# Performance work log

Measured on AMD Instinct MI355X. Metric: run time of the kernel, lower is better.

## Reference

```python
import jax, jax.numpy as jnp
import numpy as np

B, N, D = 2, 4096, 1152   # batch, tokens, txt_dim == pix_dim (num_heads = 1)
RMS_EPS = 1e-8


def setup_inputs() -> dict:
    key = jax.random.key(0)
    ks = jax.random.split(key, 8)
    w = lambda k, shape: jax.random.normal(k, shape, dtype=jnp.float32) * 0.02
    return {
        "x": jax.random.normal(ks[0], (B, N, D), dtype=jnp.float32),
        "c": jax.random.normal(ks[1], (B, N, D), dtype=jnp.float32),
        "Wqkv_pix": w(ks[2], (3 * D, D)),      # nn.Linear(pix_dim, 3*pix_dim), no bias
        "Wqkv_text": w(ks[3], (3 * D, D)),     # nn.Linear(txt_dim, 3*txt_dim), no bias
        "sq_text": jnp.ones((D,), jnp.float32),
        "sk_text": jnp.ones((D,), jnp.float32),
        "sq_pix": jnp.ones((D,), jnp.float32),
        "sk_pix": jnp.ones((D,), jnp.float32),
        "Wproj_pix": w(ks[4], (D, 2 * D)),     # nn.Linear(dim, txt_dim)
        "bproj_pix": jnp.zeros((D,), jnp.float32),
        "Wproj_text": w(ks[5], (D, 2 * D)),    # nn.Linear(dim, pix_dim)
        "bproj_text": jnp.zeros((D,), jnp.float32),
    }


def _rms_norm(t, scale):
    # RMSNorm with p<0 path: L2 norm over last dim, rms = ||x|| * d^-0.5
    d = t.shape[-1]
    rms = jnp.linalg.norm(t, axis=-1, keepdims=True) * (d ** -0.5)
    return scale * (t / (rms + RMS_EPS))


def reference(x, c, Wqkv_pix, Wqkv_text, sq_text, sk_text, sq_pix, sk_pix,
              Wproj_pix, bproj_pix, Wproj_text, bproj_text):
    Bx, Nx, D1 = x.shape  # num_heads == 1, so (B, 1, N, d) == (B, N, d)
    # pix stream QKV (from x)
    qkv_pix = (x @ Wqkv_pix.T).reshape(Bx, Nx, 3, D1)
    q_pix, k_pix, v_pix = qkv_pix[:, :, 0], qkv_pix[:, :, 1], qkv_pix[:, :, 2]
    q_pix = _rms_norm(q_pix, sq_pix)
    k_pix = _rms_norm(k_pix, sk_pix)
    # text stream QKV: NOTE the original code applies qkv_text to x, not c
    qkv_text = (x @ Wqkv_text.T).reshape(Bx, Nx, 3, D1)
    q_text, k_text, v_text = qkv_text[:, :, 0], qkv_text[:, :, 1], qkv_text[:, :, 2]
    q_text = _rms_norm(q_text, sq_text)
    k_text = _rms_norm(k_text, sk_text)
    # concat text/pix along feature dim -> (B, N, 2D)
    q = jnp.concatenate([q_text, q_pix], axis=-1)
    k = jnp.concatenate([k_text, k_pix], axis=-1)
    v = jnp.concatenate([v_text, v_pix], axis=-1)
    scale = (2 * D1) ** -0.5  # head_dim = (txt_dim + pix_dim) / num_heads
    attn = jax.nn.softmax(jnp.einsum("bnd,bmd->bnm", q, k) * scale, axis=-1)
    z = jnp.einsum("bnm,bmd->bnd", attn, v)  # (B, N, 2D)
    x_out = z @ Wproj_pix.T + bproj_pix
    c_out = z @ Wproj_text.T + bproj_text
    return (x_out, c_out)
```

## Files before the change

kernel.cpp:

```cpp
#include <hip/hip_runtime.h>
#include <hip/hip_bf16.h>
#include <stdint.h>

using short8 = __attribute__((ext_vector_type(8))) short;
using f32x4  = __attribute__((ext_vector_type(4))) float;

#define DD 1152
#define ROW 6912

static __device__ __forceinline__ float bf2f(uint32_t h){
  union { uint32_t u; float f; } v; v.u = (h & 0xffffu) << 16; return v.f;
}
static __device__ __forceinline__ ushort f2bf(float f){
  union { float f; uint32_t u; } v; v.f = f;
  uint32_t r = (v.u + 0x7fffu + ((v.u >> 16) & 1u)) >> 16;
  return (ushort)r;
}
static __device__ __forceinline__ uint32_t pack2(float a, float b){
  return (uint32_t)f2bf(a) | ((uint32_t)f2bf(b) << 16);
}

static __device__ __forceinline__ void gload16(const void* g, void* l){
  __builtin_amdgcn_global_load_lds(
      (const __attribute__((address_space(1))) void*)g,
      (__attribute__((address_space(3))) void*)l, 16, 0, 0);
}

template<int EPI>
__global__ __launch_bounds__(512, 2)
void gemm256(const ushort* __restrict__ A, int lda,
             const ushort* __restrict__ Bm, int ldb,
             void* __restrict__ Cout, int ldc,
             int K, float alpha, int ntx, int row0,
             float* __restrict__ out0, float* __restrict__ out1,
             const float* __restrict__ bias0, const float* __restrict__ bias1)
{
  __shared__ __align__(16) ushort lds[65536];
  const int tid  = threadIdx.x;
  const int w    = tid >> 6, lane = tid & 63;
  const int wr   = w >> 2, wc = w & 3;

  const int nwg = gridDim.x;
  const int wg  = blockIdx.x;
  const int swz = (wg & 7) * (nwg >> 3) + (wg >> 3);
  const int tx = swz % ntx, ty = swz / ntx;
  const int m0 = ty * 256, n0 = tx * 256;

  const int srow = lane >> 2;
  const int scol = 8 * ((lane & 3) ^ ((lane >> 3) & 3));
  const int sgA  = w * 2;
  const ushort* gA0 = A  + (size_t)(m0 + sgA * 16 + srow) * lda + scol;
  const ushort* gA1 = gA0 + (size_t)16 * lda;
  const ushort* gB0 = Bm + (size_t)(n0 + sgA * 16 + srow) * ldb + scol;
  const ushort* gB1 = gB0 + (size_t)16 * ldb;

  auto stage = [&](int t, int bf) {
    ushort* Lb = lds + bf * 16384;
    gload16(gA0 + t * 32, Lb + sgA * 512);
    gload16(gA1 + t * 32, Lb + sgA * 512 + 512);
    gload16(gB0 + t * 32, Lb + 8192 + sgA * 512);
    gload16(gB1 + t * 32, Lb + 8192 + sgA * 512 + 512);
  };

  const int kq    = lane >> 4;
  const int rowA0 = wr * 128 + (lane & 15);
  const int adA   = rowA0 * 32 + 8 * (kq ^ ((rowA0 >> 1) & 3));
  const int rowB0 = wc * 64 + (lane & 15);
  const int adB   = rowB0 * 32 + 8 * (kq ^ ((rowB0 >> 1) & 3));

  f32x4 acc[8][4];
#pragma unroll
  for (int m = 0; m < 8; m++)
#pragma unroll
    for (int n = 0; n < 4; n++) acc[m][n] = f32x4{0.f, 0.f, 0.f, 0.f};

  const int nt = K >> 5;

  stage(0, 0); stage(1, 1); stage(2, 2);
  asm volatile("s_waitcnt vmcnt(8)" ::: "memory");
  __builtin_amdgcn_s_barrier();

  for (int t = 0; t < nt; ++t) {
    const ushort* Lb = lds + (t & 3) * 16384;
    short8 a[8], b[4];
#pragma unroll
    for (int m = 0; m < 8; m++) a[m] = *(const short8*)(Lb + adA + m * 512);
#pragma unroll
    for (int n = 0; n < 4; n++) b[n] = *(const short8*)(Lb + 8192 + adB + n * 512);

    if (t + 3 < nt) stage(t + 3, (t + 3) & 3);

    __builtin_amdgcn_s_setprio(1);
#pragma unroll
    for (int m = 0; m < 8; m++)
#pragma unroll
      for (int n = 0; n < 4; n++)
        acc[m][n] = __builtin_amdgcn_mfma_f32_16x16x32_bf16(a[m], b[n], acc[m][n], 0, 0, 0);
    __builtin_amdgcn_s_setprio(0);

    if      (t + 3 < nt) asm volatile("s_waitcnt vmcnt(8)" ::: "memory");
    else if (t + 2 < nt) asm volatile("s_waitcnt vmcnt(4)" ::: "memory");
    else                 asm volatile("s_waitcnt vmcnt(0)" ::: "memory");
    __builtin_amdgcn_s_barrier();
  }

#pragma unroll
  for (int m = 0; m < 8; m++) {
#pragma unroll
    for (int v = 0; v < 4; v++) {
      const int row = m0 + wr * 128 + m * 16 + (lane >> 4) * 4 + v;
#pragma unroll
      for (int n = 0; n < 4; n++) {
        const int col = n0 + wc * 64 + n * 16 + (lane & 15);
        float val = acc[m][n][v] * alpha;
        if (EPI == 0) {
          ((ushort*)Cout)[(size_t)row * ldc + col] = f2bf(val);
        } else {
          const int orow = row0 + row;
          if (col < DD) out0[(size_t)orow * DD + col] = val + bias0[col];
          else          out1[(size_t)orow * DD + (col - DD)] = val + bias1[col - DD];
        }
      }
    }
  }
}

__global__ __launch_bounds__(256)
void cvt_f32_bf16(const float* __restrict__ src, ushort* __restrict__ dst, int n4)
{
  int stride = gridDim.x * blockDim.x;
  for (int i = blockIdx.x * blockDim.x + threadIdx.x; i < n4; i += stride) {
    float4 v = ((const float4*)src)[i];
    uint2 o;
    o.x = pack2(v.x, v.y);
    o.y = pack2(v.z, v.w);
    ((uint2*)dst)[i] = o;
  }
}

__global__ __launch_bounds__(256)
void rms_inplace(ushort* __restrict__ qkv,
                 const float* __restrict__ sq_text, const float* __restrict__ sq_pix,
                 const float* __restrict__ sk_text, const float* __restrict__ sk_pix)
{
  const int row = blockIdx.x;
  const int tid = threadIdx.x, wave = tid >> 6, lane = tid & 63;
  ushort* seg = qkv + (size_t)row * ROW + wave * 1152;
  const float* scale = (wave == 0) ? sq_text : (wave == 1) ? sq_pix
                     : (wave == 2) ? sk_text : sk_pix;
  float ss = 0.f;
  for (int g = lane; g < 144; g += 64) {
    uint4 p = *(const uint4*)(seg + g * 8);
    float f0 = bf2f(p.x), f1 = bf2f(p.x >> 16), f2 = bf2f(p.y), f3 = bf2f(p.y >> 16);
    float f4 = bf2f(p.z), f5 = bf2f(p.z >> 16), f6 = bf2f(p.w), f7 = bf2f(p.w >> 16);
    ss += f0*f0 + f1*f1 + f2*f2 + f3*f3 + f4*f4 + f5*f5 + f6*f6 + f7*f7;
  }
#pragma unroll
  for (int off = 32; off; off >>= 1) ss += __shfl_xor(ss, off);
  float rms = sqrtf(ss) * 0.0294627825f;
  float inv = 1.0f / (rms + 1e-8f);
  for (int g = lane; g < 144; g += 64) {
    int d0 = g * 8;
    uint4 p = *(const uint4*)(seg + d0);
    float f[8];
    f[0]=bf2f(p.x); f[1]=bf2f(p.x>>16); f[2]=bf2f(p.y); f[3]=bf2f(p.y>>16);
    f[4]=bf2f(p.z); f[5]=bf2f(p.z>>16); f[6]=bf2f(p.w); f[7]=bf2f(p.w>>16);
    uint4 o;
    o.x = pack2(f[0]*scale[d0+0]*inv, f[1]*scale[d0+1]*inv);
    o.y = pack2(f[2]*scale[d0+2]*inv, f[3]*scale[d0+3]*inv);
    o.z = pack2(f[4]*scale[d0+4]*inv, f[5]*scale[d0+5]*inv);
    o.w = pack2(f[6]*scale[d0+6]*inv, f[7]*scale[d0+7]*inv);
    *(uint4*)(seg + d0) = o;
  }
}

__global__ __launch_bounds__(256)
void transpose_v(const ushort* __restrict__ qkv, ushort* __restrict__ Vt)
{
  __shared__ ushort t[64][72];
  const int nb = blockIdx.x, db = blockIdx.y, b = blockIdx.z;
  const int tid = threadIdx.x;
  const int d0 = db * 64;
  const int srccol = 4608 + d0;
  const int rr = tid >> 3, cc = (tid & 7) * 8;
#pragma unroll
  for (int it = 0; it < 2; it++) {
    int r = rr + it * 32;
    uint4 p = *(const uint4*)(qkv + (size_t)(b * 4096 + nb * 64 + r) * ROW + srccol + cc);
    *(uint4*)&t[r][cc] = p;
  }
  __syncthreads();
#pragma unroll
  for (int it = 0; it < 2; it++) {
    int d = rr + it * 32;
    uint4 o;
    o.x = (uint32_t)t[cc+0][d] | ((uint32_t)t[cc+1][d] << 16);
    o.y = (uint32_t)t[cc+2][d] | ((uint32_t)t[cc+3][d] << 16);
    o.z = (uint32_t)t[cc+4][d] | ((uint32_t)t[cc+5][d] << 16);
    o.w = (uint32_t)t[cc+6][d] | ((uint32_t)t[cc+7][d] << 16);
    *(uint4*)(Vt + ((size_t)b * 2304 + d0 + d) * 4096 + nb * 64 + cc) = o;
  }
}

__global__ __launch_bounds__(256)
void softmax_bf16(ushort* __restrict__ S)
{
  const int row = blockIdx.x;
  ushort* sr = S + (size_t)row * 4096;
  const int tid = threadIdx.x, wave = tid >> 6, lane = tid & 63;
  __shared__ float red[8];
  uint4 p0 = ((const uint4*)sr)[tid * 2];
  uint4 p1 = ((const uint4*)sr)[tid * 2 + 1];
  float f[16];
  f[0]=bf2f(p0.x); f[1]=bf2f(p0.x>>16); f[2]=bf2f(p0.y); f[3]=bf2f(p0.y>>16);
  f[4]=bf2f(p0.z); f[5]=bf2f(p0.z>>16); f[6]=bf2f(p0.w); f[7]=bf2f(p0.w>>16);
  f[8]=bf2f(p1.x); f[9]=bf2f(p1.x>>16); f[10]=bf2f(p1.y); f[11]=bf2f(p1.y>>16);
  f[12]=bf2f(p1.z); f[13]=bf2f(p1.z>>16); f[14]=bf2f(p1.w); f[15]=bf2f(p1.w>>16);
  float mx = f[0];
#pragma unroll
  for (int j = 1; j < 16; j++) mx = fmaxf(mx, f[j]);
#pragma unroll
  for (int off = 32; off; off >>= 1) mx = fmaxf(mx, __shfl_xor(mx, off));
  if (lane == 0) red[wave] = mx;
  __syncthreads();
  mx = fmaxf(fmaxf(red[0], red[1]), fmaxf(red[2], red[3]));
  float s = 0.f;
#pragma unroll
  for (int j = 0; j < 16; j++) { f[j] = expf(f[j] - mx); s += f[j]; }
#pragma unroll
  for (int off = 32; off; off >>= 1) s += __shfl_xor(s, off);
  if (lane == 0) red[4 + wave] = s;
  __syncthreads();
  s = red[4] + red[5] + red[6] + red[7];
  float inv = 1.0f / s;
  uint4 o0, o1;
  o0.x = pack2(f[0]*inv, f[1]*inv);  o0.y = pack2(f[2]*inv, f[3]*inv);
  o0.z = pack2(f[4]*inv, f[5]*inv);  o0.w = pack2(f[6]*inv, f[7]*inv);
  o1.x = pack2(f[8]*inv, f[9]*inv);  o1.y = pack2(f[10]*inv, f[11]*inv);
  o1.z = pack2(f[12]*inv, f[13]*inv); o1.w = pack2(f[14]*inv, f[15]*inv);
  ((uint4*)sr)[tid * 2]     = o0;
  ((uint4*)sr)[tid * 2 + 1] = o1;
}

extern "C" void kernel_launch(void* const* d_in, const int* in_sizes, int n_in,
                              void* d_out, int out_size, void* d_ws, size_t ws_size,
                              hipStream_t stream)
{
  const float* x          = (const float*)d_in[0];
  const float* Wqkv_pix   = (const float*)d_in[2];
  const float* Wqkv_text  = (const float*)d_in[3];
  const float* sq_text    = (const float*)d_in[4];
  const float* sk_text    = (const float*)d_in[5];
  const float* sq_pix     = (const float*)d_in[6];
  const float* sk_pix     = (const float*)d_in[7];
  const float* Wproj_pix  = (const float*)d_in[8];
  const float* bproj_pix  = (const float*)d_in[9];
  const float* Wproj_text = (const float*)d_in[10];
  const float* bproj_text = (const float*)d_in[11];

  if (ws_size < 195166208ULL) return;
  char* ws = (char*)d_ws;
  ushort* QKV = (ushort*)(ws);
  ushort* Z   = (ushort*)(ws);
  ushort* Vt  = (ushort*)(ws + 113246208);
  ushort* S   = (ushort*)(ws + 150994944);
  ushort* Wpb = (ushort*)(ws + 184549376);
  ushort* xb  = (ushort*)(ws + 113246208);
  ushort* Wb  = (ushort*)(ws + 150994944);

  cvt_f32_bf16<<<2048, 256, 0, stream>>>(x, xb, 9437184 / 4);
  for (int t = 0; t < 3; t++) {
    cvt_f32_bf16<<<512, 256, 0, stream>>>(Wqkv_text + (size_t)t * 1327104,
                                          Wb + (size_t)(2 * t) * 1327104, 1327104 / 4);
    cvt_f32_bf16<<<512, 256, 0, stream>>>(Wqkv_pix + (size_t)t * 1327104,
                                          Wb + (size_t)(2 * t + 1) * 1327104, 1327104 / 4);
  }
  cvt_f32_bf16<<<512, 256, 0, stream>>>(Wproj_pix, Wpb, 2654208 / 4);
  cvt_f32_bf16<<<512, 256, 0, stream>>>(Wproj_text, Wpb + 2654208, 2654208 / 4);

  gemm256<0><<<dim3(864), 512, 0, stream>>>(xb, 1152, Wb, 1152, QKV, ROW,
                                            1152, 1.0f, 27, 0,
                                            nullptr, nullptr, nullptr, nullptr);
  rms_inplace<<<8192, 256, 0, stream>>>(QKV, sq_text, sq_pix, sk_text, sk_pix);
  {
    dim3 g(64, 36, 2);
    transpose_v<<<g, 256, 0, stream>>>(QKV, Vt);
  }

  const float scale = 1.0f / 48.0f;
  const size_t slab = (size_t)4096 * ROW;
  for (int b = 0; b < 2; b++) {
    const ushort* Qb = QKV + b * slab;
    const ushort* Kb = QKV + b * slab + 2304;
    const ushort* Vb = Vt + (size_t)b * 2304 * 4096;
    ushort* Zb = Z + (size_t)b * 4096 * 2304;
    gemm256<0><<<dim3(256), 512, 0, stream>>>(Qb, ROW, Kb, ROW, S, 4096,
                                              2304, scale, 16, 0,
                                              nullptr, nullptr, nullptr, nullptr);
    softmax_bf16<<<4096, 256, 0, stream>>>(S);
    gemm256<0><<<dim3(144), 512, 0, stream>>>(S, 4096, Vb, 4096, Zb, 2304,
                                              4096, 1.0f, 9, 0,
                                              nullptr, nullptr, nullptr, nullptr);
  }

  {
    float* out0 = (float*)d_out;
    float* out1 = out0 + 9437184;
    gemm256<2><<<dim3(288), 512, 0, stream>>>(Z, 2304, Wpb, 2304, nullptr, 0,
                                              2304, 1.0f, 9, 0,
                                              out0, out1, bproj_pix, bproj_text);
  }
}
```

Measured before the change: 761.5 us.

## Split GEMM main loop into two phases interleaving LDS reads, loads and MFMAs

The GEMM inner loop is split into two halves. Each half issues part of the global-to-LDS prefetch and part of the A-fragment LDS reads, then runs half of the MFMA block, so memory traffic overlaps with matrix math more finely. An extra workgroup barrier per iteration is added to line the phases up. That barrier adds synchronisation cost, and overlap only helps if the scheduler does not already hide the loads.

```diff
diff --git a/kernel.cpp b/kernel.cpp
--- a/kernel.cpp
+++ b/kernel.cpp
@@ -54,7 +54,7 @@
   const ushort* gB0 = Bm + (size_t)(n0 + sgA * 16 + srow) * ldb + scol;
   const ushort* gB1 = gB0 + (size_t)16 * ldb;
 
-  auto stage = [&](int t, int bf) {
+  auto stageAll = [&](int t, int bf) {
     ushort* Lb = lds + bf * 16384;
     gload16(gA0 + t * 32, Lb + sgA * 512);
     gload16(gA1 + t * 32, Lb + sgA * 512 + 512);
@@ -76,32 +76,50 @@
 
   const int nt = K >> 5;
 
-  stage(0, 0); stage(1, 1); stage(2, 2);
+  stageAll(0, 0); stageAll(1, 1); stageAll(2, 2);
   asm volatile("s_waitcnt vmcnt(8)" ::: "memory");
   __builtin_amdgcn_s_barrier();
 
   for (int t = 0; t < nt; ++t) {
     const ushort* Lb = lds + (t & 3) * 16384;
-    short8 a[8], b[4];
-#pragma unroll
-    for (int m = 0; m < 8; m++) a[m] = *(const short8*)(Lb + adA + m * 512);
+    short8 a0[4], b[4];
+#pragma unroll
+    for (int m = 0; m < 4; m++) a0[m] = *(const short8*)(Lb + adA + m * 512);
 #pragma unroll
     for (int n = 0; n < 4; n++) b[n] = *(const short8*)(Lb + 8192 + adB + n * 512);
-
-    if (t + 3 < nt) stage(t + 3, (t + 3) & 3);
-
+    if (t + 3 < nt) {
+      ushort* Ld = lds + ((t + 3) & 3) * 16384;
+      gload16(gA0 + (t + 3) * 32, Ld + sgA * 512);
+      gload16(gA1 + (t + 3) * 32, Ld + sgA * 512 + 512);
+    }
+    __builtin_amdgcn_s_barrier();
     __builtin_amdgcn_s_setprio(1);
 #pragma unroll
-    for (int m = 0; m < 8; m++)
+    for (int m = 0; m < 4; m++)
 #pragma unroll
       for (int n = 0; n < 4; n++)
-        acc[m][n] = __builtin_amdgcn_mfma_f32_16x16x32_bf16(a[m], b[n], acc[m][n], 0, 0, 0);
+        acc[m][n] = __builtin_amdgcn_mfma_f32_16x16x32_bf16(a0[m], b[n], acc[m][n], 0, 0, 0);
     __builtin_amdgcn_s_setprio(0);
 
+    short8 a1[4];
+#pragma unroll
+    for (int m = 0; m < 4; m++) a1[m] = *(const short8*)(Lb + adA + (m + 4) * 512);
+    if (t + 3 < nt) {
+      ushort* Ld = lds + ((t + 3) & 3) * 16384;
+      gload16(gB0 + (t + 3) * 32, Ld + 8192 + sgA * 512);
+      gload16(gB1 + (t + 3) * 32, Ld + 8192 + sgA * 512 + 512);
+    }
     if      (t + 3 < nt) asm volatile("s_waitcnt vmcnt(8)" ::: "memory");
     else if (t + 2 < nt) asm volatile("s_waitcnt vmcnt(4)" ::: "memory");
     else                 asm volatile("s_waitcnt vmcnt(0)" ::: "memory");
     __builtin_amdgcn_s_barrier();
+    __builtin_amdgcn_s_setprio(1);
+#pragma unroll
+    for (int m = 0; m < 4; m++)
+#pragma unroll
+      for (int n = 0; n < 4; n++)
+        acc[m + 4][n] = __builtin_amdgcn_mfma_f32_16x16x32_bf16(a1[m], b[n], acc[m + 4][n], 0, 0, 0);
+    __builtin_amdgcn_s_setprio(0);
   }
 
 #pragma unroll
```

Result: no change. 755.3 us (-0.8%).

## Shrink GEMM tile to 256x128, double-buffer LDS fragments, batch PV GEMM

Applied to the files above, without the earlier changes.

Shrinks the GEMM tile from 256x256 to 256x128 so each of the 8 waves owns a 64x64 sub-tile. The LDS-to-register fragment loads are now prefetched one k-step ahead in ping-pong register buffers. The workspace is re-laid out so both batches' score matrices live in separate buffers, which lets the two PV GEMMs run as one batched launch via blockIdx.y strides. The smaller tile raises workgroup counts and improves CU occupancy on the small attention GEMMs (144/256 tiles before). The cost is lower arithmetic intensity per tile, and the loop assumes an even number of k-steps.

```diff
diff --git a/kernel.cpp b/kernel.cpp
--- a/kernel.cpp
+++ b/kernel.cpp
@@ -28,93 +28,102 @@
 
 template<int EPI>
 __global__ __launch_bounds__(512, 2)
-void gemm256(const ushort* __restrict__ A, int lda,
-             const ushort* __restrict__ Bm, int ldb,
-             void* __restrict__ Cout, int ldc,
-             int K, float alpha, int ntx, int row0,
-             float* __restrict__ out0, float* __restrict__ out1,
-             const float* __restrict__ bias0, const float* __restrict__ bias1)
-{
-  __shared__ __align__(16) ushort lds[65536];
+void gemmRP(const ushort* __restrict__ A, int lda, long long sA,
+            const ushort* __restrict__ Bm, int ldb, long long sB,
+            void* __restrict__ Cout, int ldc, long long sC,
+            int K, float alpha, int ntx, int row0,
+            float* __restrict__ out0, float* __restrict__ out1,
+            const float* __restrict__ bias0, const float* __restrict__ bias1)
+{
+  __shared__ __align__(16) ushort lds[49152];
   const int tid  = threadIdx.x;
   const int w    = tid >> 6, lane = tid & 63;
-  const int wr   = w >> 2, wc = w & 3;
+  const int wr   = w >> 1, wc = w & 1;
+
+  A  += (long long)blockIdx.y * sA;
+  Bm += (long long)blockIdx.y * sB;
 
   const int nwg = gridDim.x;
   const int wg  = blockIdx.x;
   const int swz = (wg & 7) * (nwg >> 3) + (wg >> 3);
   const int tx = swz % ntx, ty = swz / ntx;
-  const int m0 = ty * 256, n0 = tx * 256;
+  const int m0 = ty * 256, n0 = tx * 128;
 
   const int srow = lane >> 2;
   const int scol = 8 * ((lane & 3) ^ ((lane >> 3) & 3));
-  const int sgA  = w * 2;
-  const ushort* gA0 = A  + (size_t)(m0 + sgA * 16 + srow) * lda + scol;
+  const ushort* gA0 = A  + (size_t)(m0 + (2 * w) * 16 + srow) * lda + scol;
   const ushort* gA1 = gA0 + (size_t)16 * lda;
-  const ushort* gB0 = Bm + (size_t)(n0 + sgA * 16 + srow) * ldb + scol;
-  const ushort* gB1 = gB0 + (size_t)16 * ldb;
+  const ushort* gB0 = Bm + (size_t)(n0 + w * 16 + srow) * ldb + scol;
 
   auto stage = [&](int t, int bf) {
-    ushort* Lb = lds + bf * 16384;
-    gload16(gA0 + t * 32, Lb + sgA * 512);
-    gload16(gA1 + t * 32, Lb + sgA * 512 + 512);
-    gload16(gB0 + t * 32, Lb + 8192 + sgA * 512);
-    gload16(gB1 + t * 32, Lb + 8192 + sgA * 512 + 512);
+    ushort* Lb = lds + bf * 12288;
+    gload16(gA0 + t * 32, Lb + (2 * w) * 512);
+    gload16(gA1 + t * 32, Lb + (2 * w) * 512 + 512);
+    gload16(gB0 + t * 32, Lb + 8192 + w * 512);
   };
 
-  const int kq    = lane >> 4;
-  const int rowA0 = wr * 128 + (lane & 15);
-  const int adA   = rowA0 * 32 + 8 * (kq ^ ((rowA0 >> 1) & 3));
-  const int rowB0 = wc * 64 + (lane & 15);
-  const int adB   = rowB0 * 32 + 8 * (kq ^ ((rowB0 >> 1) & 3));
-
-  f32x4 acc[8][4];
-#pragma unroll
-  for (int m = 0; m < 8; m++)
+  const int kq   = lane >> 4;
+  const int rowA = wr * 64 + (lane & 15);
+  const int adA  = rowA * 32 + 8 * (kq ^ ((rowA >> 1) & 3));
+  const int rowB = wc * 64 + (lane & 15);
+  const int adB  = 8192 + rowB * 32 + 8 * (kq ^ ((rowB >> 1) & 3));
+
+  f32x4 acc[4][4];
+#pragma unroll
+  for (int m = 0; m < 4; m++)
 #pragma unroll
     for (int n = 0; n < 4; n++) acc[m][n] = f32x4{0.f, 0.f, 0.f, 0.f};
 
   const int nt = K >> 5;
 
+  short8 aP[4], bP[4], aQ[4], bQ[4];
+
   stage(0, 0); stage(1, 1); stage(2, 2);
-  asm volatile("s_waitcnt vmcnt(8)" ::: "memory");
+  asm volatile("s_waitcnt vmcnt(3)" ::: "memory");
   __builtin_amdgcn_s_barrier();
-
-  for (int t = 0; t < nt; ++t) {
-    const ushort* Lb = lds + (t & 3) * 16384;
-    short8 a[8], b[4];
-#pragma unroll
-    for (int m = 0; m < 8; m++) a[m] = *(const short8*)(Lb + adA + m * 512);
-#pragma unroll
-    for (int n = 0; n < 4; n++) b[n] = *(const short8*)(Lb + 8192 + adB + n * 512);
-
+#pragma unroll
+  for (int m = 0; m < 4; m++) aP[m] = *(const short8*)(lds + adA + m * 512);
+#pragma unroll
+  for (int n = 0; n < 4; n++) bP[n] = *(const short8*)(lds + adB + n * 512);
+
+  auto iter = [&](int t, short8 (&CA)[4], short8 (&CB)[4],
+                         short8 (&NA)[4], short8 (&NB)[4]) {
+    if (t + 1 < nt) {
+      const ushort* Lb = lds + ((t + 1) & 3) * 12288;
+#pragma unroll
+      for (int m = 0; m < 4; m++) NA[m] = *(const short8*)(Lb + adA + m * 512);
+#pragma unroll
+      for (int n = 0; n < 4; n++) NB[n] = *(const short8*)(Lb + adB + n * 512);
+    }
     if (t + 3 < nt) stage(t + 3, (t + 3) & 3);
-
     __builtin_amdgcn_s_setprio(1);
 #pragma unroll
-    for (int m = 0; m < 8; m++)
+    for (int m = 0; m < 4; m++)
 #pragma unroll
       for (int n = 0; n < 4; n++)
-        acc[m][n] = __builtin_amdgcn_mfma_f32_16x16x32_bf16(a[m], b[n], acc[m][n], 0, 0, 0);
+        acc[m][n] = __builtin_amdgcn_mfma_f32_16x16x32_bf16(CA[m], CB[n], acc[m][n], 0, 0, 0);
     __builtin_amdgcn_s_setprio(0);
-
-    if      (t + 3 < nt) asm volatile("s_waitcnt vmcnt(8)" ::: "memory");
-    else if (t + 2 < nt) asm volatile("s_waitcnt vmcnt(4)" ::: "memory");
-    else                 asm volatile("s_waitcnt vmcnt(0)" ::: "memory");
+    if (t + 3 < nt) asm volatile("s_waitcnt vmcnt(3)" ::: "memory");
+    else            asm volatile("s_waitcnt vmcnt(0)" ::: "memory");
     __builtin_amdgcn_s_barrier();
-  }
-
-#pragma unroll
-  for (int m = 0; m < 8; m++) {
+  };
+
+  for (int t = 0; t < nt; t += 2) {
+    iter(t,     aP, bP, aQ, bQ);
+    iter(t + 1, aQ, bQ, aP, bP);
+  }
+
+#pragma unroll
+  for (int m = 0; m < 4; m++) {
 #pragma unroll
     for (int v = 0; v < 4; v++) {
-      const int row = m0 + wr * 128 + m * 16 + (lane >> 4) * 4 + v;
+      const int row = m0 + wr * 64 + m * 16 + (lane >> 4) * 4 + v;
 #pragma unroll
       for (int n = 0; n < 4; n++) {
         const int col = n0 + wc * 64 + n * 16 + (lane & 15);
         float val = acc[m][n][v] * alpha;
         if (EPI == 0) {
-          ((ushort*)Cout)[(size_t)row * ldc + col] = f2bf(val);
+          ((ushort*)Cout)[(long long)blockIdx.y * sC + (size_t)row * ldc + col] = f2bf(val);
         } else {
           const int orow = row0 + row;
           if (col < DD) out0[(size_t)orow * DD + col] = val + bias0[col];
@@ -261,9 +270,10 @@
   if (ws_size < 195166208ULL) return;
   char* ws = (char*)d_ws;
   ushort* QKV = (ushort*)(ws);
-  ushort* Z   = (ushort*)(ws);
+  ushort* S1  = (ushort*)(ws);
+  ushort* Z   = (ushort*)(ws + 33554432);
   ushort* Vt  = (ushort*)(ws + 113246208);
-  ushort* S   = (ushort*)(ws + 150994944);
+  ushort* S0  = (ushort*)(ws + 150994944);
   ushort* Wpb = (ushort*)(ws + 184549376);
   ushort* xb  = (ushort*)(ws + 113246208);
   ushort* Wb  = (ushort*)(ws + 150994944);
@@ -278,8 +288,8 @@
   cvt_f32_bf16<<<512, 256, 0, stream>>>(Wproj_pix, Wpb, 2654208 / 4);
   cvt_f32_bf16<<<512, 256, 0, stream>>>(Wproj_text, Wpb + 2654208, 2654208 / 4);
 
-  gemm256<0><<<dim3(864), 512, 0, stream>>>(xb, 1152, Wb, 1152, QKV, ROW,
-                                            1152, 1.0f, 27, 0,
+  gemmRP<0><<<dim3(1728), 512, 0, stream>>>(xb, 1152, 0, Wb, 1152, 0, QKV, ROW, 0,
+                                            1152, 1.0f, 54, 0,
                                             nullptr, nullptr, nullptr, nullptr);
   rms_inplace<<<8192, 256, 0, stream>>>(QKV, sq_text, sq_pix, sk_text, sk_pix);
   {
@@ -289,25 +299,30 @@
 
   const float scale = 1.0f / 48.0f;
   const size_t slab = (size_t)4096 * ROW;
-  for (int b = 0; b < 2; b++) {
-    const ushort* Qb = QKV + b * slab;
-    const ushort* Kb = QKV + b * slab + 2304;
-    const ushort* Vb = Vt + (size_t)b * 2304 * 4096;
-    ushort* Zb = Z + (size_t)b * 4096 * 2304;
-    gemm256<0><<<dim3(256), 512, 0, stream>>>(Qb, ROW, Kb, ROW, S, 4096,
-                                              2304, scale, 16, 0,
-                                              nullptr, nullptr, nullptr, nullptr);
-    softmax_bf16<<<4096, 256, 0, stream>>>(S);
-    gemm256<0><<<dim3(144), 512, 0, stream>>>(S, 4096, Vb, 4096, Zb, 2304,
-                                              4096, 1.0f, 9, 0,
-                                              nullptr, nullptr, nullptr, nullptr);
+
+  gemmRP<0><<<dim3(512), 512, 0, stream>>>(QKV, ROW, 0, QKV + 2304, ROW, 0,
+                                           S0, 4096, 0, 2304, scale, 32, 0,
+                                           nullptr, nullptr, nullptr, nullptr);
+  softmax_bf16<<<4096, 256, 0, stream>>>(S0);
+  gemmRP<0><<<dim3(512), 512, 0, stream>>>(QKV + slab, ROW, 0, QKV + slab + 2304, ROW, 0,
+                                           S1, 4096, 0, 2304, scale, 32, 0,
+                                           nullptr, nullptr, nullptr, nullptr);
+  softmax_bf16<<<4096, 256, 0, stream>>>(S1);
+
+  {
+    long long sAb = (long long)(S1 - S0);
+    long long sBb = (long long)2304 * 4096;
+    long long sCb = (long long)4096 * 2304;
+    gemmRP<0><<<dim3(288, 2), 512, 0, stream>>>(S0, 4096, sAb, Vt, 4096, sBb,
+                                                Z, 2304, sCb, 4096, 1.0f, 18, 0,
+                                                nullptr, nullptr, nullptr, nullptr);
   }
 
   {
     float* out0 = (float*)d_out;
     float* out1 = out0 + 9437184;
-    gemm256<2><<<dim3(288), 512, 0, stream>>>(Z, 2304, Wpb, 2304, nullptr, 0,
-                                              2304, 1.0f, 9, 0,
-                                              out0, out1, bproj_pix, bproj_text);
-  }
-}
+    gemmRP<2><<<dim3(576), 512, 0, stream>>>(Z, 2304, 0, Wpb, 2304, 0, nullptr, 0, 0,
+                                             2304, 1.0f, 18, 0,
+                                             out0, out1, bproj_pix, bproj_text);
+  }
+}
```

New measurement: 805.4 us. +5.8%, slower.
